# Kernel tuning notes

Measured on AMD Instinct MI355X. Metric: run time of the kernel, lower is better.

## Reference

```python
import jax, jax.numpy as jnp
import numpy as np
import math

N_HEADS = 16
STRIDE = 4
LN_EPS = 1e-5
ROPE_BASE = 10000.0


def rotate_half(x):
    h = x.shape[-1] // 2
    return jnp.concatenate([-x[..., h:], x[..., :h]], axis=-1)


def rope_cos_sin(seq_len, head_dim, dtype):
    inv_freq = 1.0 / (ROPE_BASE ** (jnp.arange(0, head_dim, 2, dtype=jnp.float32) / head_dim))
    t = jnp.arange(seq_len, dtype=jnp.float32)
    freqs = jnp.outer(t, inv_freq)                      # [S, hd/2]
    emb = jnp.concatenate([freqs, freqs], axis=-1)      # [S, hd]
    return jnp.cos(emb).astype(dtype), jnp.sin(emb).astype(dtype)


def linear_upsample(x, T):
    # x: [B, Ts, D] -> [B, T, D]; matches F.interpolate(mode='linear', align_corners=False)
    Ts = x.shape[1]
    scale = Ts / T
    src = (jnp.arange(T, dtype=jnp.float32) + 0.5) * scale - 0.5
    src = jnp.clip(src, 0.0, Ts - 1.0)
    i0 = jnp.floor(src).astype(jnp.int32)
    i1 = jnp.minimum(i0 + 1, Ts - 1)
    w = (src - i0.astype(jnp.float32)).astype(x.dtype)[None, :, None]
    return x[:, i0, :] * (1.0 - w) + x[:, i1, :] * w


def setup_inputs() -> dict:
    key = jax.random.key(0)
    ks = jax.random.split(key, 4)
    B, T, D = 4, 4096, 1024
    s = 1.0 / math.sqrt(D)
    return {
        "x": jax.random.normal(ks[0], (B, T, D), dtype=jnp.float32),
        "norm_w": jnp.ones((D,), dtype=jnp.float32),
        "norm_b": jnp.zeros((D,), dtype=jnp.float32),
        "W_qkv": jax.random.normal(ks[1], (D, 3 * D), dtype=jnp.float32) * s,
        "b_qkv": jnp.zeros((3 * D,), dtype=jnp.float32),
        "W_out": jax.random.normal(ks[2], (D, D), dtype=jnp.float32) * s,
        "b_out": jnp.zeros((D,), dtype=jnp.float32),
    }


def reference(x, norm_w, norm_b, W_qkv, b_qkv, W_out, b_out):
    B, T, D = x.shape
    H = N_HEADS
    hd = D // H
    residual = x

    # LayerNorm (biased variance, eps=1e-5)
    mu = jnp.mean(x, axis=-1, keepdims=True)
    var = jnp.var(x, axis=-1, keepdims=True)
    x_norm = (x - mu) * jax.lax.rsqrt(var + LN_EPS) * norm_w + norm_b

    # strided downsample (T >= 2*stride path)
    xs = x_norm[:, ::STRIDE, :]
    Ts = xs.shape[1]

    # fused QKV projection
    qkv = xs @ W_qkv + b_qkv                             # [B, Ts, 3D]
    qkv = qkv.reshape(B, Ts, 3, H, hd).transpose(2, 0, 3, 1, 4)
    q, k, v = qkv[0], qkv[1], qkv[2]                     # [B, H, Ts, hd]

    # RoPE
    cos, sin = rope_cos_sin(Ts, hd, q.dtype)             # [Ts, hd]
    q = q * cos + rotate_half(q) * sin
    k = k * cos + rotate_half(k) * sin

    # causal SDPA on strided subsequence
    scores = jnp.einsum('bhqd,bhkd->bhqk', q, k) / math.sqrt(hd)
    causal = jnp.tril(jnp.ones((Ts, Ts), dtype=bool))
    scores = jnp.where(causal, scores, jnp.finfo(scores.dtype).min)
    attn = jax.nn.softmax(scores, axis=-1)
    out = jnp.einsum('bhqk,bhkd->bhqd', attn, v)         # [B, H, Ts, hd]
    out = out.transpose(0, 2, 1, 3).reshape(B, Ts, D)

    out = out @ W_out + b_out
    out = linear_upsample(out, T)                        # [B, T, D]
    return residual + out
```

## Files before the change

kernel.cpp:

```cpp
#include <hip/hip_runtime.h>
#include <hip/hip_bf16.h>

#define DEVFN __device__ __forceinline__

typedef float f32x4 __attribute__((ext_vector_type(4)));
typedef float f32x16 __attribute__((ext_vector_type(16)));
typedef __bf16 bf16x8 __attribute__((ext_vector_type(8)));
typedef unsigned short u16x8 __attribute__((ext_vector_type(8)));
typedef unsigned short u16x4 __attribute__((ext_vector_type(4)));
typedef unsigned u32x4 __attribute__((ext_vector_type(4)));

DEVFN unsigned short f2bf(float f) {
  unsigned u = __builtin_bit_cast(unsigned, f);
  u = (u + 0x7FFFu + ((u >> 16) & 1u)) >> 16;
  return (unsigned short)u;
}

DEVFN f32x4 mfma_bf16(u16x8 a, u16x8 b, f32x4 c) {
  return __builtin_amdgcn_mfma_f32_16x16x32_bf16((bf16x8)a, (bf16x8)b, c, 0, 0, 0);
}

DEVFN f32x16 mfma32(u16x8 a, u16x8 b, f32x16 c) {
  return __builtin_amdgcn_mfma_f32_32x32x16_bf16((bf16x8)a, (bf16x8)b, c, 0, 0, 0);
}

DEVFN unsigned cvt_pk_bf16(float a, float b) {
  unsigned r;
  asm("v_cvt_pk_bf16_f32 %0, %1, %2" : "=v"(r) : "v"(a), "v"(b));
  return r;
}

DEVFN void permswap(unsigned& a, unsigned& b) {
  asm("v_permlane32_swap_b32 %0, %1" : "+v"(a), "+v"(b));
}

DEVFN void sincos_rev(float rev, float* sn, float* cs) {
  float fr, s, c;
  asm("v_fract_f32 %0, %1" : "=v"(fr) : "v"(rev));
  asm("v_sin_f32 %0, %1" : "=v"(s) : "v"(fr));
  asm("v_cos_f32 %0, %1" : "=v"(c) : "v"(fr));
  *sn = s; *cs = c;
}

DEVFN void gload_lds16(const void* g, void* l) {
  __builtin_amdgcn_global_load_lds(
      (const __attribute__((address_space(1))) void*)g,
      (__attribute__((address_space(3))) void*)l, 16, 0, 0);
}

__global__ __launch_bounds__(256) void ln_stride_kernel(
    const float* __restrict__ x, const float* __restrict__ w,
    const float* __restrict__ bb, unsigned short* __restrict__ xs,
    int T, int Ts, int D, int stride) {
  int row = blockIdx.x;
  int b = row / Ts, ts = row - b * Ts;
  const float* xr = x + ((size_t)b * T + (size_t)ts * stride) * D;
  int t = threadIdx.x;
  float4 v = *(const float4*)(xr + t * 4);
  float s = v.x + v.y + v.z + v.w;
  float sq = v.x * v.x + v.y * v.y + v.z * v.z + v.w * v.w;
#pragma unroll
  for (int m = 1; m < 64; m <<= 1) { s += __shfl_xor(s, m); sq += __shfl_xor(sq, m); }
  __shared__ float ps[4], pq[4];
  if ((t & 63) == 0) { ps[t >> 6] = s; pq[t >> 6] = sq; }
  __syncthreads();
  s = ps[0] + ps[1] + ps[2] + ps[3];
  sq = pq[0] + pq[1] + pq[2] + pq[3];
  float invD = 1.0f / (float)D;
  float mu = s * invD;
  float var = sq * invD - mu * mu;
  float rs = rsqrtf(var + 1e-5f);
  int c = t * 4;
  float4 wv = *(const float4*)(w + c);
  float4 bv = *(const float4*)(bb + c);
  u16x4 o;
  o[0] = f2bf((v.x - mu) * rs * wv.x + bv.x);
  o[1] = f2bf((v.y - mu) * rs * wv.y + bv.y);
  o[2] = f2bf((v.z - mu) * rs * wv.z + bv.z);
  o[3] = f2bf((v.w - mu) * rs * wv.w + bv.w);
  *(u16x4*)(xs + (size_t)row * D + c) = o;
}

__global__ __launch_bounds__(256) void wconv_kernel(
    const float* __restrict__ W, unsigned short* __restrict__ Wt, int K, int N) {
  __shared__ float tile[32][33];
  int n0 = blockIdx.x * 32, k0 = blockIdx.y * 32;
  int tx = threadIdx.x & 31, ty = threadIdx.x >> 5;
#pragma unroll
  for (int i = 0; i < 32; i += 8) tile[ty + i][tx] = W[(size_t)(k0 + ty + i) * N + n0 + tx];
  __syncthreads();
#pragma unroll
  for (int i = 0; i < 32; i += 8) Wt[(size_t)(n0 + ty + i) * K + k0 + tx] = f2bf(tile[tx][ty + i]);
}

__global__ __launch_bounds__(512, 1) void gemm_qkv256_kernel(
    const unsigned short* __restrict__ A, const unsigned short* __restrict__ Bt,
    const float* __restrict__ bias, int M, int N, int Kd,
    unsigned short* __restrict__ Qo, unsigned short* __restrict__ Ko,
    unsigned short* __restrict__ Vt) {
  __shared__ __align__(128) char lds[131072];
  const int tid = threadIdx.x, l = tid & 63, w = tid >> 6;
  const int wr = w >> 2, wc = w & 3;
  const int lg = l >> 4, lr = l & 15;
  const int o = blockIdx.x;
  const int xcd = o & 7, s = o >> 3;
  const int bm = (xcd & 3) * 4 + (s & 3);
  const int bn = (xcd >> 2) * 6 + (s >> 2);
  const int m0 = bm << 8, n0 = bn << 8;
  const int chk = (lg ^ ((lr >> 1) & 3)) << 4;

  f32x4 acc[8][4] = {};

#define STAGE32(kk, bufoff)                                                 \
  do {                                                                      \
    _Pragma("unroll")                                                       \
    for (int i_ = 0; i_ < 2; i_++) {                                        \
      int c_ = tid + (i_ << 9);                                             \
      int rl_ = c_ >> 2, c4_ = c_ & 3;                                      \
      int cs_ = c4_ ^ ((rl_ >> 1) & 3);                                     \
      gload_lds16(A + (size_t)(m0 + rl_) * Kd + (kk) + cs_ * 8,             \
                  lds + (bufoff) + c_ * 16);                                \
      gload_lds16(Bt + (size_t)(n0 + rl_) * Kd + (kk) + cs_ * 8,            \
                  lds + (bufoff) + 16384 + c_ * 16);                        \
    }                                                                       \
  } while (0)

  STAGE32(0, 0);
  STAGE32(32, 32768);
  STAGE32(64, 65536);

  const int NT = Kd >> 5;
  for (int t = 0; t < NT; ++t) {
    if (t < NT - 2)       asm volatile("s_waitcnt vmcnt(8)" ::: "memory");
    else if (t == NT - 2) asm volatile("s_waitcnt vmcnt(4)" ::: "memory");
    else                  asm volatile("s_waitcnt vmcnt(0)" ::: "memory");
    __builtin_amdgcn_s_barrier();
    const int curoff = (t & 3) << 15;

    u16x8 bfr[4], afr[8];
#pragma unroll
    for (int nf = 0; nf < 4; nf++)
      bfr[nf] = *(const u16x8*)(lds + curoff + 16384 +
                                (wc * 64 + nf * 16 + lr) * 64 + chk);
#pragma unroll
    for (int mf = 0; mf < 8; mf++)
      afr[mf] = *(const u16x8*)(lds + curoff +
                                (wr * 128 + mf * 16 + lr) * 64 + chk);
    if (t + 3 < NT) STAGE32((t + 3) << 5, ((t + 3) & 3) << 15);
    asm volatile("s_waitcnt lgkmcnt(0)" ::: "memory");
    __builtin_amdgcn_sched_barrier(0);
    __builtin_amdgcn_s_setprio(1);
#pragma unroll
    for (int mf = 0; mf < 8; mf++)
#pragma unroll
      for (int nf = 0; nf < 4; nf++)
        acc[mf][nf] = mfma_bf16(afr[mf], bfr[nf], acc[mf][nf]);
    __builtin_amdgcn_s_setprio(0);
    __builtin_amdgcn_s_barrier();
  }
#undef STAGE32

  int nb = n0 + wc * 64;
  int which = nb >> 10;
  int h = (nb & 1023) >> 6;
  if (which < 2) {
    unsigned short* dst = (which == 0) ? Qo : Ko;
    float qsc = (which == 0) ? 0.18033688f : 1.0f;
#pragma unroll
    for (int nt = 0; nt < 2; nt++) {
      int d = nt * 16 + lr;
      float invf_rev = exp2f((float)d * -0.41524101f) * 0.15915494f;
      float blo = bias[nb + nt * 16 + lr];
      float bhi = bias[nb + (nt + 2) * 16 + lr];
#pragma unroll
      for (int mt = 0; mt < 8; mt++) {
        int mb = m0 + wr * 128 + mt * 16 + lg * 4;
#pragma unroll
        for (int r = 0; r < 4; r++) {
          int m = mb + r;
          int b_ = m >> 10, ts = m & 1023;
          float va = acc[mt][nt][r] + blo;
          float vb = acc[mt][nt + 2][r] + bhi;
          float sn, cs;
          sincos_rev((float)ts * invf_rev, &sn, &cs);
          size_t base = (((size_t)(b_ * 16 + h)) * 1024 + ts) * 64;
          dst[base + d] = f2bf((va * cs - vb * sn) * qsc);
          dst[base + d + 32] = f2bf((vb * cs + va * sn) * qsc);
        }
      }
    }
  } else {
#pragma unroll
    for (int nt = 0; nt < 4; nt++) {
      int d = nt * 16 + lr;
      float bi = bias[nb + nt * 16 + lr];
#pragma unroll
      for (int mt = 0; mt < 8; mt++) {
        int mb = m0 + wr * 128 + mt * 16 + lg * 4;
        int b_ = mb >> 10, tsb = mb & 1023;
        u16x4 pk;
#pragma unroll
        for (int r = 0; r < 4; r++) pk[r] = f2bf(acc[mt][nt][r] + bi);
        *(u16x4*)(Vt + (size_t)(b_ * 16 + h) * 65536 +
                  (size_t)(tsb >> 5) * 2048 + d * 32 + (tsb & 31)) = pk;
      }
    }
  }
}

__global__ __launch_bounds__(256) void gemm_out_kernel(
    const unsigned short* __restrict__ A, const unsigned short* __restrict__ Bt,
    const float* __restrict__ bias, int M, int N, int Kd,
    float* __restrict__ Co) {
  constexpr int BK = 32;
  __shared__ unsigned short As[2][128 * BK];
  __shared__ unsigned short Bs[2][128 * BK];
  int nbm = M >> 7;
  int bm = blockIdx.x % nbm, bn = blockIdx.x / nbm;
  int m0 = bm << 7, n0 = bn << 7;
  int t = threadIdx.x, l = t & 63, w = t >> 6;
  int wr = w >> 1, wc = w & 1;
  int lg = l >> 4, lr = l & 15;

  f32x4 acc[4][4] = {};
  int srow = t >> 2, scol = (t & 3) * 8;
  const unsigned short* gA = A + (size_t)(m0 + srow) * Kd + scol;
  const unsigned short* gB = Bt + (size_t)(n0 + srow) * Kd + scol;

#define STAGE_G(buf, kk)                                          \
  do {                                                            \
    unsigned short* la_ = &As[buf][t * 8];                        \
    unsigned short* lb_ = &Bs[buf][t * 8];                        \
    gload_lds16(gA + (kk), la_);                                  \
    gload_lds16(gA + (kk) + (size_t)64 * Kd, la_ + 64 * BK);      \
    gload_lds16(gB + (kk), lb_);                                  \
    gload_lds16(gB + (kk) + (size_t)64 * Kd, lb_ + 64 * BK);      \
  } while (0)

  STAGE_G(0, 0);
  __syncthreads();
  int cur = 0;
  for (int k0 = 0; k0 < Kd; k0 += BK) {
    bool more = (k0 + BK < Kd);
    if (more) STAGE_G(cur ^ 1, k0 + BK);
    u16x8 af[4], bf[4];
#pragma unroll
    for (int i = 0; i < 4; i++) {
      af[i] = *(const u16x8*)(&As[cur][(wr * 64 + i * 16 + lr) * BK + lg * 8]);
      bf[i] = *(const u16x8*)(&Bs[cur][(wc * 64 + i * 16 + lr) * BK + lg * 8]);
    }
#pragma unroll
    for (int i = 0; i < 4; i++)
#pragma unroll
      for (int j = 0; j < 4; j++) acc[i][j] = mfma_bf16(af[i], bf[j], acc[i][j]);
    if (more) __syncthreads();
    cur ^= 1;
  }
#undef STAGE_G

#pragma unroll
  for (int nt = 0; nt < 4; nt++) {
    int n = n0 + wc * 64 + nt * 16 + lr;
    float bi = bias[n];
#pragma unroll
    for (int mt = 0; mt < 4; mt++) {
      int mb = m0 + wr * 64 + mt * 16 + lg * 4;
#pragma unroll
      for (int r = 0; r < 4; r++) Co[(size_t)(mb + r) * N + n] = acc[mt][nt][r] + bi;
    }
  }
}

__global__ __launch_bounds__(256) void attn_kernel(
    const unsigned short* __restrict__ Q, const unsigned short* __restrict__ K,
    const unsigned short* __restrict__ Vt, unsigned short* __restrict__ O,
    int Ts, int H) {
  __shared__ __align__(128) char kvlds[2][16384];
  int t = threadIdx.x, w = t >> 6, l = t & 63;
  int h2 = l >> 5, lq = l & 31;
  int bh = blockIdx.x & 63;
  int i = blockIdx.x >> 6;
  int qg = (i < 4) ? 7 - i : i - 4;
  int b = bh / H, hh = bh % H;
  int qw0 = qg * 128 + w * 32;

  const unsigned short* Qh = Q + ((size_t)bh * Ts) * 64;
  const unsigned short* Kh = K + ((size_t)bh * Ts) * 64;
  const unsigned short* Vh = Vt + (size_t)bh * 65536;

  u16x8 qf[4];
#pragma unroll
  for (int c = 0; c < 4; c++)
    qf[c] = *(const u16x8*)(Qh + (size_t)(qw0 + lq) * 64 + c * 16 + h2 * 8);

#define STAGE_KV(jt, buf)                                                   \
  do {                                                                      \
    _Pragma("unroll")                                                       \
    for (int i_ = 0; i_ < 2; i_++) {                                        \
      int c_ = t + (i_ << 8);                                               \
      int r_ = c_ >> 3, jg_ = c_ & 7;                                       \
      gload_lds16(Kh + (size_t)(jt) * 4096 + r_ * 64 + ((jg_ ^ (r_ & 7)) << 3), \
                  kvlds[buf] + c_ * 16);                                    \
    }                                                                       \
    {                                                                       \
      int d_ = t >> 2, g_ = t & 3;                                          \
      int gs_ = (g_ ^ ((d_ >> 1) & 3)) << 3;                                \
      gload_lds16(Vh + (size_t)(2 * (jt)) * 2048 + d_ * 32 + gs_,           \
                  kvlds[buf] + 8192 + t * 16);                              \
      gload_lds16(Vh + (size_t)(2 * (jt) + 1) * 2048 + d_ * 32 + gs_,       \
                  kvlds[buf] + 12288 + t * 16);                             \
    }                                                                       \
  } while (0)

  f32x16 olo = {}, ohi = {};
  float mrow = -1e30f, lsum = 0.f;
  const int sk = lq & 7;
  const int sv = (lq >> 1) & 3;

  int ntiles = 2 * qg + 2;
  STAGE_KV(0, 0);

  for (int jt = 0; jt < ntiles; jt++) {
    __syncthreads();
    int cur = jt & 1;
    if (jt + 1 < ntiles) STAGE_KV(jt + 1, cur ^ 1);

    int kvt = jt * 64;
    if (kvt > qw0) continue;
    bool haveS1 = (kvt + 32 <= qw0);
    bool diag0 = (kvt == qw0);
    bool diag1 = (kvt + 32 == qw0);

    const char* kb0 = kvlds[cur] + lq * 128;
    const char* kb1 = kvlds[cur] + (32 + lq) * 128;
    u16x8 kf0[4], kf1[4];
#pragma unroll
    for (int c = 0; c < 4; c++)
      kf0[c] = *(const u16x8*)(kb0 + (((c << 1) + h2) ^ sk) * 16);
    f32x16 sA = {}, sB = {};
    if (haveS1) {
#pragma unroll
      for (int c = 0; c < 4; c++)
        kf1[c] = *(const u16x8*)(kb1 + (((c << 1) + h2) ^ sk) * 16);
      __builtin_amdgcn_s_setprio(1);
#pragma unroll
      for (int c = 0; c < 4; c++) sA = mfma32(kf0[c], qf[c], sA);
#pragma unroll
      for (int c = 0; c < 4; c++) sB = mfma32(kf1[c], qf[c], sB);
      __builtin_amdgcn_s_setprio(0);
    } else {
      __builtin_amdgcn_s_setprio(1);
#pragma unroll
      for (int c = 0; c < 4; c++) sA = mfma32(kf0[c], qf[c], sA);
      __builtin_amdgcn_s_setprio(0);
    }

    float p[32];
#pragma unroll
    for (int r = 0; r < 16; r++) {
      float v = sA[r];
      if (diag0) {
        int kvl = (r & 3) + 8 * (r >> 2) + 4 * h2;
        v = (kvl > lq) ? -1e30f : v;
      }
      p[r] = v;
    }
#pragma unroll
    for (int r = 0; r < 16; r++) {
      float v = haveS1 ? sB[r] : -1e30f;
      if (diag1) {
        int kvl = (r & 3) + 8 * (r >> 2) + 4 * h2;
        v = (kvl > lq) ? -1e30f : v;
      }
      p[16 + r] = v;
    }

    float m16[16], m8[8], m4[4];
#pragma unroll
    for (int r = 0; r < 16; r++) m16[r] = fmaxf(p[r], p[16 + r]);
#pragma unroll
    for (int r = 0; r < 8; r++) m8[r] = fmaxf(m16[r], m16[r + 8]);
#pragma unroll
    for (int r = 0; r < 4; r++) m4[r] = fmaxf(m8[r], m8[r + 4]);
    float tmax = fmaxf(fmaxf(m4[0], m4[2]), fmaxf(m4[1], m4[3]));
    tmax = fmaxf(tmax, __shfl_xor(tmax, 32));

    if (!__all(tmax <= mrow + 8.0f)) {
      float mnew = fmaxf(mrow, tmax);
      float al = exp2f(mrow - mnew);
      mrow = mnew;
      lsum *= al;
      olo *= al;
      ohi *= al;
    }

#pragma unroll
    for (int r = 0; r < 32; r++) p[r] = exp2f(p[r] - mrow);
    float s16[16], s8[8], s4[4];
#pragma unroll
    for (int r = 0; r < 16; r++) s16[r] = p[r] + p[16 + r];
#pragma unroll
    for (int r = 0; r < 8; r++) s8[r] = s16[r] + s16[r + 8];
#pragma unroll
    for (int r = 0; r < 4; r++) s4[r] = s8[r] + s8[r + 4];
    lsum += (s4[0] + s4[2]) + (s4[1] + s4[3]);

    {
      unsigned a01 = cvt_pk_bf16(p[0], p[1]),   a23 = cvt_pk_bf16(p[2], p[3]);
      unsigned a45 = cvt_pk_bf16(p[4], p[5]),   a67 = cvt_pk_bf16(p[6], p[7]);
      unsigned a89 = cvt_pk_bf16(p[8], p[9]),   aAB = cvt_pk_bf16(p[10], p[11]);
      unsigned aCD = cvt_pk_bf16(p[12], p[13]), aEF = cvt_pk_bf16(p[14], p[15]);
      permswap(a01, a45);
      permswap(a23, a67);
      permswap(a89, aCD);
      permswap(aAB, aEF);
      u32x4 f0 = {a01, a23, a45, a67};
      u32x4 f1 = {a89, aAB, aCD, aEF};
      u16x8 P0 = __builtin_bit_cast(u16x8, f0);
      u16x8 P1 = __builtin_bit_cast(u16x8, f1);

      const char* vb_ = kvlds[cur] + 8192;
      u16x8 vf[4];
      vf[0] = *(const u16x8*)(vb_ + lq * 64 + ((0 + h2) ^ sv) * 16);
      vf[1] = *(const u16x8*)(vb_ + lq * 64 + ((2 + h2) ^ sv) * 16);
      vf[2] = *(const u16x8*)(vb_ + (32 + lq) * 64 + ((0 + h2) ^ sv) * 16);
      vf[3] = *(const u16x8*)(vb_ + (32 + lq) * 64 + ((2 + h2) ^ sv) * 16);
      __builtin_amdgcn_s_setprio(1);
      olo = mfma32(vf[0], P0, olo);
      olo = mfma32(vf[1], P1, olo);
      ohi = mfma32(vf[2], P0, ohi);
      ohi = mfma32(vf[3], P1, ohi);
      __builtin_amdgcn_s_setprio(0);
    }

    if (haveS1) {
      unsigned b01 = cvt_pk_bf16(p[16], p[17]), b23 = cvt_pk_bf16(p[18], p[19]);
      unsigned b45 = cvt_pk_bf16(p[20], p[21]), b67 = cvt_pk_bf16(p[22], p[23]);
      unsigned b89 = cvt_pk_bf16(p[24], p[25]), bAB = cvt_pk_bf16(p[26], p[27]);
      unsigned bCD = cvt_pk_bf16(p[28], p[29]), bEF = cvt_pk_bf16(p[30], p[31]);
      permswap(b01, b45);
      permswap(b23, b67);
      permswap(b89, bCD);
      permswap(bAB, bEF);
      u32x4 g0 = {b01, b23, b45, b67};
      u32x4 g1 = {b89, bAB, bCD, bEF};
      u16x8 Q0 = __builtin_bit_cast(u16x8, g0);
      u16x8 Q1 = __builtin_bit_cast(u16x8, g1);

      const char* vb_ = kvlds[cur] + 8192 + 4096;
      u16x8 vf[4];
      vf[0] = *(const u16x8*)(vb_ + lq * 64 + ((0 + h2) ^ sv) * 16);
      vf[1] = *(const u16x8*)(vb_ + lq * 64 + ((2 + h2) ^ sv) * 16);
      vf[2] = *(const u16x8*)(vb_ + (32 + lq) * 64 + ((0 + h2) ^ sv) * 16);
      vf[3] = *(const u16x8*)(vb_ + (32 + lq) * 64 + ((2 + h2) ^ sv) * 16);
      __builtin_amdgcn_s_setprio(1);
      olo = mfma32(vf[0], Q0, olo);
      olo = mfma32(vf[1], Q1, olo);
      ohi = mfma32(vf[2], Q0, ohi);
      ohi = mfma32(vf[3], Q1, ohi);
      __builtin_amdgcn_s_setprio(0);
    }
  }
#undef STAGE_KV

  lsum += __shfl_xor(lsum, 32);
  float inv = 1.0f / lsum;
  int q = qw0 + lq;
  unsigned short* orow = O + ((size_t)b * Ts + q) * (size_t)(H * 64) + hh * 64;
#pragma unroll
  for (int g = 0; g < 4; g++) {
    u16x4 plo, phi;
#pragma unroll
    for (int j2 = 0; j2 < 4; j2++) {
      plo[j2] = f2bf(olo[g * 4 + j2] * inv);
      phi[j2] = f2bf(ohi[g * 4 + j2] * inv);
    }
    *(u16x4*)(orow + g * 8 + h2 * 4) = plo;
    *(u16x4*)(orow + 32 + g * 8 + h2 * 4) = phi;
  }
}

__global__ __launch_bounds__(256) void upsample_kernel(
    const float* __restrict__ x, const float* __restrict__ proj,
    float* __restrict__ out, int T, int Ts, int D) {
  int bk = blockIdx.x;
  int b = bk / Ts, k = bk - b * Ts;
  int d4 = threadIdx.x;
  size_t prow = (size_t)b * Ts * D;
  const f32x4 a = *((const f32x4*)(proj + prow + (size_t)max(k - 1, 0) * D) + d4);
  const f32x4 bb = *((const f32x4*)(proj + prow + (size_t)k * D) + d4);
  const f32x4 c = *((const f32x4*)(proj + prow + (size_t)min(k + 1, Ts - 1) * D) + d4);

  size_t xbase = ((size_t)b * T + 4 * (size_t)k) * D + (size_t)d4 * 4;
  f32x4 x0 = __builtin_nontemporal_load((const f32x4*)(x + xbase));
  f32x4 x1 = __builtin_nontemporal_load((const f32x4*)(x + xbase + D));
  f32x4 x2 = __builtin_nontemporal_load((const f32x4*)(x + xbase + 2 * D));
  f32x4 x3 = __builtin_nontemporal_load((const f32x4*)(x + xbase + 3 * D));

  f32x4 o0 = x0 + 0.375f * a + 0.625f * bb;
  f32x4 o1 = x1 + 0.125f * a + 0.875f * bb;
  f32x4 o2 = x2 + 0.875f * bb + 0.125f * c;
  f32x4 o3 = x3 + 0.625f * bb + 0.375f * c;

  __builtin_nontemporal_store(o0, (f32x4*)(out + xbase));
  __builtin_nontemporal_store(o1, (f32x4*)(out + xbase + D));
  __builtin_nontemporal_store(o2, (f32x4*)(out + xbase + 2 * D));
  __builtin_nontemporal_store(o3, (f32x4*)(out + xbase + 3 * D));
}

extern "C" void kernel_launch(void* const* d_in, const int* in_sizes, int n_in,
                              void* d_out, int out_size, void* d_ws, size_t ws_size,
                              hipStream_t stream) {
  (void)in_sizes; (void)n_in; (void)out_size; (void)ws_size;
  const float* x = (const float*)d_in[0];
  const float* norm_w = (const float*)d_in[1];
  const float* norm_b = (const float*)d_in[2];
  const float* W_qkv = (const float*)d_in[3];
  const float* b_qkv = (const float*)d_in[4];
  const float* W_out = (const float*)d_in[5];
  const float* b_out = (const float*)d_in[6];
  float* out = (float*)d_out;

  const int B = 4, T = 4096, D = 1024, H = 16, STR = 4;
  const int Ts = T / STR;
  const int M = B * Ts;

  char* ws = (char*)d_ws;
  unsigned short* xs  = (unsigned short*)(ws);
  unsigned short* Wtq = (unsigned short*)(ws + ((size_t)8 << 20));
  unsigned short* Wto = (unsigned short*)(ws + ((size_t)14 << 20));
  unsigned short* Qb  = (unsigned short*)(ws + ((size_t)16 << 20));
  unsigned short* Kb  = (unsigned short*)(ws + ((size_t)24 << 20));
  unsigned short* Vtb = (unsigned short*)(ws + ((size_t)32 << 20));
  float* proj         = (float*)(ws + ((size_t)16 << 20));
  unsigned short* att = xs;

  ln_stride_kernel<<<M, 256, 0, stream>>>(x, norm_w, norm_b, xs, T, Ts, D, STR);
  wconv_kernel<<<dim3(3 * D / 32, D / 32), 256, 0, stream>>>(W_qkv, Wtq, D, 3 * D);
  wconv_kernel<<<dim3(D / 32, D / 32), 256, 0, stream>>>(W_out, Wto, D, D);
  gemm_qkv256_kernel<<<(M / 256) * (3 * D / 256), 512, 0, stream>>>(
      xs, Wtq, b_qkv, M, 3 * D, D, Qb, Kb, Vtb);
  attn_kernel<<<B * H * 8, 256, 0, stream>>>(Qb, Kb, Vtb, att, Ts, H);
  gemm_out_kernel<<<(M / 128) * (D / 128), 256, 0, stream>>>(
      att, Wto, b_out, M, D, D, proj);
  upsample_kernel<<<B * Ts, 256, 0, stream>>>(x, proj, out, T, Ts, D);
}
```

Before: 141.7 us.

## Triple-buffer output GEMM with swizzled LDS, XCD-aware tile mapping and priority hints

Rewrites the output-projection GEMM main loop to use a 3-stage LDS ring with two tiles prefetched ahead, gated by explicit vmcnt waits instead of a full sync per step. It adds an XOR swizzle on the LDS chunk layout to avoid bank conflicts, remaps block indices so that M-tiles sharing an XCD are grouped for L2 reuse, and raises wave priority around the MFMA block. The intent is to hide global load latency and reduce LDS conflicts. In exchange it uses more LDS per block, and the block mapping hard-codes the M tile count (32 tiles across 8 XCDs), which could reduce occupancy or break for other shapes.

```diff
diff --git a/kernel.cpp b/kernel.cpp
--- a/kernel.cpp
+++ b/kernel.cpp
@@ -212,51 +212,64 @@
     const unsigned short* __restrict__ A, const unsigned short* __restrict__ Bt,
     const float* __restrict__ bias, int M, int N, int Kd,
     float* __restrict__ Co) {
-  constexpr int BK = 32;
-  __shared__ unsigned short As[2][128 * BK];
-  __shared__ unsigned short Bs[2][128 * BK];
-  int nbm = M >> 7;
-  int bm = blockIdx.x % nbm, bn = blockIdx.x / nbm;
-  int m0 = bm << 7, n0 = bn << 7;
-  int t = threadIdx.x, l = t & 63, w = t >> 6;
-  int wr = w >> 1, wc = w & 1;
-  int lg = l >> 4, lr = l & 15;
+  __shared__ __align__(128) char lds[49152];
+  const int tid = threadIdx.x, l = tid & 63, w = tid >> 6;
+  const int wr = w >> 1, wc = w & 1;
+  const int lg = l >> 4, lr = l & 15;
+  const int o = blockIdx.x;
+  const int xcd = o & 7, s = o >> 3;
+  const int bm = xcd * 4 + (s & 3);
+  const int bn = s >> 2;
+  const int m0 = bm << 7, n0 = bn << 7;
+  const int chk = (lg ^ ((lr >> 1) & 3)) << 4;
+
+#define STAGE32O(kk, bufoff)                                                \
+  do {                                                                      \
+    _Pragma("unroll")                                                       \
+    for (int i_ = 0; i_ < 2; i_++) {                                        \
+      int c_ = tid + (i_ << 8);                                             \
+      int rl_ = c_ >> 2, c4_ = c_ & 3;                                      \
+      int cs_ = c4_ ^ ((rl_ >> 1) & 3);                                     \
+      gload_lds16(A + (size_t)(m0 + rl_) * Kd + (kk) + cs_ * 8,             \
+                  lds + (bufoff) + c_ * 16);                                \
+      gload_lds16(Bt + (size_t)(n0 + rl_) * Kd + (kk) + cs_ * 8,            \
+                  lds + (bufoff) + 8192 + c_ * 16);                         \
+    }                                                                       \
+  } while (0)
 
   f32x4 acc[4][4] = {};
-  int srow = t >> 2, scol = (t & 3) * 8;
-  const unsigned short* gA = A + (size_t)(m0 + srow) * Kd + scol;
-  const unsigned short* gB = Bt + (size_t)(n0 + srow) * Kd + scol;
-
-#define STAGE_G(buf, kk)                                          \
-  do {                                                            \
-    unsigned short* la_ = &As[buf][t * 8];                        \
-    unsigned short* lb_ = &Bs[buf][t * 8];                        \
-    gload_lds16(gA + (kk), la_);                                  \
-    gload_lds16(gA + (kk) + (size_t)64 * Kd, la_ + 64 * BK);      \
-    gload_lds16(gB + (kk), lb_);                                  \
-    gload_lds16(gB + (kk) + (size_t)64 * Kd, lb_ + 64 * BK);      \
-  } while (0)
-
-  STAGE_G(0, 0);
-  __syncthreads();
-  int cur = 0;
-  for (int k0 = 0; k0 < Kd; k0 += BK) {
-    bool more = (k0 + BK < Kd);
-    if (more) STAGE_G(cur ^ 1, k0 + BK);
-    u16x8 af[4], bf[4];
-#pragma unroll
-    for (int i = 0; i < 4; i++) {
-      af[i] = *(const u16x8*)(&As[cur][(wr * 64 + i * 16 + lr) * BK + lg * 8]);
-      bf[i] = *(const u16x8*)(&Bs[cur][(wc * 64 + i * 16 + lr) * BK + lg * 8]);
-    }
-#pragma unroll
-    for (int i = 0; i < 4; i++)
-#pragma unroll
-      for (int j = 0; j < 4; j++) acc[i][j] = mfma_bf16(af[i], bf[j], acc[i][j]);
-    if (more) __syncthreads();
-    cur ^= 1;
+  STAGE32O(0, 0);
+  STAGE32O(32, 16384);
+
+  const int NT = Kd >> 5;
+  for (int t = 0; t < NT; ++t) {
+    if (t < NT - 1) asm volatile("s_waitcnt vmcnt(4)" ::: "memory");
+    else            asm volatile("s_waitcnt vmcnt(0)" ::: "memory");
+    __builtin_amdgcn_s_barrier();
+    const int curoff = (t % 3) * 16384;
+
+    u16x8 bfr[4], afr[4];
+#pragma unroll
+    for (int nf = 0; nf < 4; nf++)
+      bfr[nf] = *(const u16x8*)(lds + curoff + 8192 +
+                                (wc * 64 + nf * 16 + lr) * 64 + chk);
+#pragma unroll
+    for (int mf = 0; mf < 4; mf++)
+      afr[mf] = *(const u16x8*)(lds + curoff +
+                                (wr * 64 + mf * 16 + lr) * 64 + chk);
+    if (t + 2 < NT) STAGE32O((t + 2) << 5, ((t + 2) % 3) * 16384);
+    asm volatile("s_waitcnt lgkmcnt(0)" ::: "memory");
+    __builtin_amdgcn_sched_barrier(0);
+    __builtin_amdgcn_s_setprio(1);
+#pragma unroll
+    for (int mf = 0; mf < 4; mf++)
+#pragma unroll
+      for (int nf = 0; nf < 4; nf++)
+        acc[mf][nf] = mfma_bf16(afr[mf], bfr[nf], acc[mf][nf]);
+    __builtin_amdgcn_s_setprio(0);
+    __builtin_amdgcn_s_barrier();
   }
-#undef STAGE_G
+#undef STAGE32O
 
 #pragma unroll
   for (int nt = 0; nt < 4; nt++) {
```

Measured after the change: 128.0 us. 9.7% less time.
